# Optimization experiments

Hardware: AMD Instinct MI355X
Metric: run time of the kernel (lower is better)

## Reference

```python
import jax, jax.numpy as jnp
import numpy as np

K = 3          # hard-coded k in Gaussian_interpolation
SIGMA = 1.0    # hard-coded sigma


def _knn_idx(original_pts, query_pts, k):
    # original_pts: [B,3,N], query_pts: [B,3,M] -> idx [B,M,k] of nearest source points
    p2 = jnp.sum(original_pts ** 2, axis=1)          # [B,N]
    q2 = jnp.sum(query_pts ** 2, axis=1)             # [B,M]
    qp = jnp.einsum('bcm,bcn->bmn', query_pts, original_pts)  # [B,M,N]
    d2 = q2[:, :, None] + p2[:, None, :] - 2.0 * qp  # squared distances [B,M,N]
    _, idx = jax.lax.top_k(-d2, k)                   # smallest distances
    return idx


def _gather_k(x, idx):
    # x: [B,C,N], idx: [B,M,k] -> [B,C,M,k]
    return jnp.take_along_axis(x[:, :, None, :], idx[:, None, :, :], axis=3)


def _gaussian_interpolation(original_pts, query_pts, feat, idx):
    # knn points and Gaussian distance weights
    knn_pts = _gather_k(original_pts, idx)                       # [B,3,M,k]
    dist_sq = jnp.sum((knn_pts - query_pts[:, :, :, None]) ** 2, axis=1)  # [B,M,k]
    weight = jnp.exp(-dist_sq / (2.0 * SIGMA ** 2))
    weight = weight / jnp.sum(weight, axis=2, keepdims=True)     # normalize over k
    knn_feat = _gather_k(feat, idx)                              # [B,C,M,k]
    return jnp.sum(knn_feat * weight[:, None, :, :], axis=-1)    # [B,C,M]


def _adaptive_max_pool1d(x, out_size):
    # x: [B, M, C] -> pool over last dim to out_size (matches F.adaptive_max_pool1d)
    C = x.shape[-1]
    i = np.arange(out_size)
    starts = np.floor(i * C / out_size).astype(np.int64)
    ends = np.ceil((i + 1) * C / out_size).astype(np.int64)
    L = int((ends - starts).max())
    idx = starts[:, None] + np.arange(L)[None, :]   # [out_size, L]
    mask = idx < ends[:, None]
    idx = np.minimum(idx, C - 1)
    g = x[..., jnp.asarray(idx)]                    # [B, M, out_size, L]
    g = jnp.where(jnp.asarray(mask)[None, None], g, -jnp.inf)
    return jnp.max(g, axis=-1)                      # [B, M, out_size]


def setup_inputs() -> dict:
    key = jax.random.key(0)
    k1, k2, k3, k4, k5 = jax.random.split(key, 5)
    B, N, M = 2, 16384, 4096
    return {
        'original_pts': jax.random.normal(k1, (B, 3, N), dtype=jnp.float32),
        'query_pts': jax.random.normal(k2, (B, 3, M), dtype=jnp.float32),
        'local_feat1': jax.random.normal(k3, (B, 128, N), dtype=jnp.float32),
        'local_feat2': jax.random.normal(k4, (B, 256, N), dtype=jnp.float32),
        'global_feats': jax.random.normal(k5, (B, 1024), dtype=jnp.float32),
    }


def reference(original_pts, query_pts, local_feat1, local_feat2, global_feats):
    M = query_pts.shape[-1]
    idx = _knn_idx(original_pts, query_pts, K)  # shared kNN for all feature maps
    interp1 = _gaussian_interpolation(original_pts, query_pts, local_feat1, idx)  # [B,C1,M]
    interp2 = _gaussian_interpolation(original_pts, query_pts, local_feat2, idx)  # [B,C2,M]
    agg_local = jnp.concatenate([interp1, interp2], axis=1)       # [B,C1+C2,M]
    # F.interpolate to size M is an identity here (sizes already match)
    gfeat = jnp.broadcast_to(global_feats[:, :, None],
                             (global_feats.shape[0], global_feats.shape[1], M))
    agg = jnp.concatenate([query_pts, agg_local, gfeat], axis=1)  # [B,Ctot,M]
    agg = jnp.transpose(agg, (0, 2, 1))                           # [B,M,Ctot]
    return _adaptive_max_pool1d(agg, M)                           # [B,M,M]
```

## Files before the change

kernel.cpp:

```cpp
#include <hip/hip_runtime.h>

#define BB 2
#define NN 16384
#define MM 4096
#define C1 128
#define C2 256
#define CF 384
#define CG 1024
#define CT 1411
#define FLTMAX 3.402823466e+38f
#define SPLIT 64
#define PTS_PER (NN / SPLIT)

__global__ __launch_bounds__(256) void p2p_fused(
    const float* __restrict__ P, const float* __restrict__ Q,
    const float* __restrict__ F1, const float* __restrict__ F2,
    const float* __restrict__ G, float* __restrict__ out)
{
    const int t  = threadIdx.x;
    const int bm = blockIdx.x;
    const int b  = bm >> 12;
    const int m  = bm & (MM - 1);

    const float* Pb = P + (size_t)b * 3 * NN;
    const float qx = Q[(size_t)b * 3 * MM + 0 * MM + m];
    const float qy = Q[(size_t)b * 3 * MM + 1 * MM + m];
    const float qz = Q[(size_t)b * 3 * MM + 2 * MM + m];
    const float q2 = __fadd_rn(__fadd_rn(__fmul_rn(qx, qx), __fmul_rn(qy, qy)),
                               __fmul_rn(qz, qz));

    float bd0 = FLTMAX, bd1 = FLTMAX, bd2 = FLTMAX;
    int   bi0 = 0x7fffffff, bi1 = 0x7fffffff, bi2 = 0x7fffffff;

    for (int n = t; n < NN; n += 256) {
        float px = Pb[n];
        float py = Pb[NN + n];
        float pz = Pb[2 * NN + n];
        float p2 = __fadd_rn(__fadd_rn(__fmul_rn(px, px), __fmul_rn(py, py)),
                             __fmul_rn(pz, pz));
        float qp = __fadd_rn(__fadd_rn(__fmul_rn(qx, px), __fmul_rn(qy, py)),
                             __fmul_rn(qz, pz));
        float d2 = __fsub_rn(__fadd_rn(q2, p2), __fadd_rn(qp, qp));
        if (d2 < bd2) {
            if (d2 < bd1) {
                if (d2 < bd0) { bd2 = bd1; bi2 = bi1; bd1 = bd0; bi1 = bi0; bd0 = d2; bi0 = n; }
                else          { bd2 = bd1; bi2 = bi1; bd1 = d2;  bi1 = n; }
            } else            { bd2 = d2;  bi2 = n; }
        }
    }

    __shared__ float sd[256][3];
    __shared__ int   si[256][3];
    sd[t][0] = bd0; sd[t][1] = bd1; sd[t][2] = bd2;
    si[t][0] = bi0; si[t][1] = bi1; si[t][2] = bi2;
    __syncthreads();

    for (int off = 128; off >= 1; off >>= 1) {
        if (t < off) {
            float A[3]  = { sd[t][0], sd[t][1], sd[t][2] };
            int   AI[3] = { si[t][0], si[t][1], si[t][2] };
            float Bv[3] = { sd[t + off][0], sd[t + off][1], sd[t + off][2] };
            int   BI[3] = { si[t + off][0], si[t + off][1], si[t + off][2] };
            float rd[3]; int ri[3];
            int pa = 0, pb = 0;
            #pragma unroll
            for (int r = 0; r < 3; r++) {
                bool ta = (A[pa] < Bv[pb]) || (A[pa] == Bv[pb] && AI[pa] < BI[pb]);
                if (ta) { rd[r] = A[pa];  ri[r] = AI[pa]; pa++; }
                else    { rd[r] = Bv[pb]; ri[r] = BI[pb]; pb++; }
            }
            sd[t][0] = rd[0]; sd[t][1] = rd[1]; sd[t][2] = rd[2];
            si[t][0] = ri[0]; si[t][1] = ri[1]; si[t][2] = ri[2];
        }
        __syncthreads();
    }

    __shared__ float wsh[3];
    __shared__ int   ish[3];
    __shared__ float agg[CT + 1];

    if (t == 0) {
        float w[3];
        #pragma unroll
        for (int k = 0; k < 3; k++) {
            int i = si[0][k];
            ish[k] = i;
            float dx = __fsub_rn(Pb[i],          qx);
            float dy = __fsub_rn(Pb[NN + i],     qy);
            float dz = __fsub_rn(Pb[2 * NN + i], qz);
            float ds = __fadd_rn(__fadd_rn(__fmul_rn(dx, dx), __fmul_rn(dy, dy)),
                                 __fmul_rn(dz, dz));
            w[k] = expf(-0.5f * ds);
        }
        float Z = __fadd_rn(__fadd_rn(w[0], w[1]), w[2]);
        wsh[0] = w[0] / Z; wsh[1] = w[1] / Z; wsh[2] = w[2] / Z;
    }
    __syncthreads();

    const int   i0 = ish[0], i1 = ish[1], i2 = ish[2];
    const float w0 = wsh[0], w1 = wsh[1], w2 = wsh[2];

    if (t < 3) agg[t] = (t == 0) ? qx : ((t == 1) ? qy : qz);

    for (int c = t; c < C1 + C2; c += 256) {
        const float* base = (c < C1)
            ? (F1 + ((size_t)b * C1 + c) * NN)
            : (F2 + ((size_t)b * C2 + (c - C1)) * NN);
        float f0 = base[i0], f1 = base[i1], f2 = base[i2];
        float v = __fadd_rn(__fadd_rn(__fmul_rn(f0, w0), __fmul_rn(f1, w1)),
                            __fmul_rn(f2, w2));
        agg[3 + c] = v;
    }
    for (int c = t; c < CG; c += 256) {
        agg[3 + C1 + C2 + c] = G[(size_t)b * CG + c];
    }
    __syncthreads();

    float* orow = out + ((size_t)b * MM + m) * MM;
    for (int j = t; j < MM; j += 256) {
        int s = (j * CT) >> 12;
        int e = ((j + 1) * CT + (MM - 1)) >> 12;
        float v = agg[s];
        if (e - s > 1) v = fmaxf(v, agg[s + 1]);
        orow[j] = v;
    }
}

__global__ __launch_bounds__(256) void prep_all(
    const float* __restrict__ P,  const float* __restrict__ F1,
    const float* __restrict__ F2, const float* __restrict__ G,
    float4* __restrict__ P4, float* __restrict__ Ft, float* __restrict__ pg)
{
    __shared__ float tile[64][65];
    const int blk = blockIdx.x;
    const int t   = threadIdx.x;

    if (blk < 3072) {
        const int b  = blk / 1536;
        const int r  = blk % 1536;
        const int ct = r / 256;
        const int nt = r % 256;
        const int c0 = ct * 64, n0 = nt * 64;
        const int tx = t & 63;
        const int ty = t >> 6;

        #pragma unroll 4
        for (int i = 0; i < 16; i++) {
            int cl = ty + i * 4;
            int c  = c0 + cl;
            const float* src = (c < C1)
                ? (F1 + ((size_t)b * C1 + c) * NN)
                : (F2 + ((size_t)b * C2 + (c - C1)) * NN);
            tile[cl][tx] = src[n0 + tx];
        }
        __syncthreads();
        #pragma unroll 4
        for (int i = 0; i < 16; i++) {
            int nl = ty + i * 4;
            Ft[((size_t)b * NN + (n0 + nl)) * CF + c0 + tx] = tile[tx][nl];
        }
    } else if (blk < 3200) {
        int gid = (blk - 3072) * 256 + t;
        int b   = gid >> 14;
        int n   = gid & (NN - 1);
        const float* Pb = P + (size_t)b * 3 * NN;
        float x = Pb[n], y = Pb[NN + n], z = Pb[2 * NN + n];
        float p2 = __fadd_rn(__fadd_rn(__fmul_rn(x, x), __fmul_rn(y, y)),
                             __fmul_rn(z, z));
        P4[gid] = make_float4(x, y, z, p2);
    } else {
        int gid = (blk - 3200) * 256 + t;
        int b   = gid / 2972;
        int jj  = gid % 2972;
        if (b < BB) {
            int j = 1124 + jj;
            int s = (j * CT) >> 12;
            int e = ((j + 1) * CT + (MM - 1)) >> 12;
            float v = G[(size_t)b * CG + (s - 387)];
            if (e - s > 1) v = fmaxf(v, G[(size_t)b * CG + (s - 386)]);
            pg[(size_t)b * MM + j] = v;
        }
    }
}

__device__ __forceinline__ float dist_rn(float qx, float qy, float qz, float q2,
                                         float4 v)
{
    float qp = __fadd_rn(__fadd_rn(__fmul_rn(qx, v.x), __fmul_rn(qy, v.y)),
                         __fmul_rn(qz, v.z));
    return __fsub_rn(__fadd_rn(q2, v.w), __fadd_rn(qp, qp));
}

#define INS(dv, nv)                                                          \
    {                                                                        \
        bool c0 = (dv) < b0, c1 = (dv) < b1, c2 = (dv) < b2;                 \
        float nb2 = c1 ? b1 : (c2 ? (dv) : b2);                              \
        int   ni2 = c1 ? i1 : (c2 ? (nv) : i2);                              \
        float nb1 = c0 ? b0 : (c1 ? (dv) : b1);                              \
        int   ni1 = c0 ? i0 : (c1 ? (nv) : i1);                              \
        float nb0 = c0 ? (dv) : b0;                                          \
        int   ni0 = c0 ? (nv) : i0;                                          \
        b0 = nb0; b1 = nb1; b2 = nb2; i0 = ni0; i1 = ni1; i2 = ni2;          \
    }

#define INSL(dv, nv)                                                         \
    {                                                                        \
        bool c0 = ((dv) < b0) || ((dv) == b0 && (nv) < i0);                  \
        bool c1 = ((dv) < b1) || ((dv) == b1 && (nv) < i1);                  \
        bool c2 = ((dv) < b2) || ((dv) == b2 && (nv) < i2);                  \
        float nb2 = c1 ? b1 : (c2 ? (dv) : b2);                              \
        int   ni2 = c1 ? i1 : (c2 ? (nv) : i2);                              \
        float nb1 = c0 ? b0 : (c1 ? (dv) : b1);                              \
        int   ni1 = c0 ? i0 : (c1 ? (nv) : i1);                              \
        float nb0 = c0 ? (dv) : b0;                                          \
        int   ni0 = c0 ? (nv) : i0;                                          \
        b0 = nb0; b1 = nb1; b2 = nb2; i0 = ni0; i1 = ni1; i2 = ni2;          \
    }

__global__ __launch_bounds__(256) void knn_scan(
    const float4* __restrict__ P4, const float* __restrict__ Q,
    float4* __restrict__ pd, int4* __restrict__ pi)
{
    const int t    = threadIdx.x;
    const int lane = t & 63;
    const int wv   = __builtin_amdgcn_readfirstlane(t >> 6);
    const int qg   = blockIdx.x & 127;
    const int ps   = blockIdx.x >> 7;
    const int sp   = ps * 4 + wv;
    const int mg   = qg * 64 + lane;
    const int b    = qg >> 6;
    const int m    = mg & (MM - 1);

    const float qx = Q[(size_t)b * 3 * MM + m];
    const float qy = Q[(size_t)b * 3 * MM + MM + m];
    const float qz = Q[(size_t)b * 3 * MM + 2 * MM + m];
    const float q2 = __fadd_rn(__fadd_rn(__fmul_rn(qx, qx), __fmul_rn(qy, qy)),
                               __fmul_rn(qz, qz));

    const float4* Pw = P4 + b * NN + sp * PTS_PER;
    const int nbase = sp * PTS_PER;

    float b0 = FLTMAX, b1 = FLTMAX, b2 = FLTMAX;
    int   i0 = 0x7fffffff, i1 = 0x7fffffff, i2 = 0x7fffffff;

    #pragma unroll 4
    for (int g = 0; g < PTS_PER; g += 4) {
        float4 v0 = Pw[g + 0];
        float4 v1 = Pw[g + 1];
        float4 v2 = Pw[g + 2];
        float4 v3 = Pw[g + 3];
        float d0  = dist_rn(qx, qy, qz, q2, v0);
        float d1  = dist_rn(qx, qy, qz, q2, v1);
        float d2v = dist_rn(qx, qy, qz, q2, v2);
        float d3  = dist_rn(qx, qy, qz, q2, v3);

        bool  cA = d1 < d0;   float mA = fminf(d0, d1);   int uA = cA ? 1 : 0;
        bool  cB = d3 < d2v;  float mB = fminf(d2v, d3);  int uB = cB ? 3 : 2;
        bool  cF = mB < mA;   float mF = fminf(mA, mB);   int uF = cF ? uB : uA;
        int nmin = nbase + g + uF;

        float MA = fmaxf(d0, d1), MB = fmaxf(d2v, d3);
        float sec = fminf(cF ? mA : mB, cF ? MB : MA);

        INS(mF, nmin);

        if (sec < b2) {
            #pragma unroll
            for (int u = 0; u < 4; u++) {
                float du = (u == 0) ? d0 : ((u == 1) ? d1 : ((u == 2) ? d2v : d3));
                if (uF != u) {
                    INS(du, nbase + g + u);
                }
            }
        }
    }

    int o = (mg << 6) + sp;
    pd[o] = make_float4(b0, b1, b2, 0.0f);
    pi[o] = make_int4(i0, i1, i2, 0);
}

__global__ __launch_bounds__(256) void merge_interp_pool(
    const float4* __restrict__ P4, const float* __restrict__ Q,
    const float* __restrict__ G, const float* __restrict__ Ft,
    const float4* __restrict__ pd, const int4* __restrict__ pi,
    const float* __restrict__ pg, float* __restrict__ out)
{
    __shared__ float agg[392];
    __shared__ float swt[3];
    __shared__ int   sidm[3];

    const int t  = threadIdx.x;
    const int mg = blockIdx.x;
    const int b  = mg >> 12;
    const int m  = mg & (MM - 1);

    float4* out4 = (float4*)(out + (size_t)mg * MM);

    if (t < 64) {
        const int lane = t;
        float4 d4 = pd[(mg << 6) + lane];
        int4   i4 = pi[(mg << 6) + lane];
        float b0 = d4.x, b1 = d4.y, b2 = d4.z;
        int   i0 = i4.x, i1 = i4.y, i2 = i4.z;

        #pragma unroll
        for (int mask = 1; mask < 64; mask <<= 1) {
            float e0 = __shfl_xor(b0, mask);
            float e1 = __shfl_xor(b1, mask);
            float e2 = __shfl_xor(b2, mask);
            int   j0 = __shfl_xor(i0, mask);
            int   j1 = __shfl_xor(i1, mask);
            int   j2 = __shfl_xor(i2, mask);
            INSL(e0, j0);
            INSL(e1, j1);
            INSL(e2, j2);
        }

        int myid = (lane == 0) ? i0 : ((lane == 1) ? i1 : i2);
        float w = 0.0f;
        if (lane < 3) {
            float qx = Q[(size_t)b * 3 * MM + m];
            float qy = Q[(size_t)b * 3 * MM + MM + m];
            float qz = Q[(size_t)b * 3 * MM + 2 * MM + m];
            float4 pv = P4[b * NN + myid];
            float dx = __fsub_rn(pv.x, qx);
            float dy = __fsub_rn(pv.y, qy);
            float dz = __fsub_rn(pv.z, qz);
            float ds = __fadd_rn(__fadd_rn(__fmul_rn(dx, dx), __fmul_rn(dy, dy)),
                                 __fmul_rn(dz, dz));
            w = expf(-0.5f * ds);
        }
        float wA = __shfl(w, 0);
        float wB = __shfl(w, 1);
        float wC = __shfl(w, 2);
        if (lane < 3) {
            float Z = __fadd_rn(__fadd_rn(wA, wB), wC);
            swt[lane]  = w / Z;
            sidm[lane] = myid;
        }
    } else {
        if (t >= 65 && t < 68) {
            agg[t - 65] = Q[(size_t)b * 3 * MM + (size_t)(t - 65) * MM + m];
        }
        if (t == 64) agg[387] = G[(size_t)b * CG];
        const float4* pg4 = (const float4*)(pg + (size_t)b * MM);
        for (int g = t - 64; g < 743; g += 192) {
            out4[281 + g] = pg4[281 + g];
        }
    }
    __syncthreads();

    const int   i0 = sidm[0], i1 = sidm[1], i2 = sidm[2];
    const float w0 = swt[0],  w1 = swt[1],  w2 = swt[2];
    const float* r0 = Ft + ((size_t)b * NN + i0) * CF;
    const float* r1 = Ft + ((size_t)b * NN + i1) * CF;
    const float* r2 = Ft + ((size_t)b * NN + i2) * CF;

    for (int c = t; c < CF; c += 256) {
        float v = __fadd_rn(__fadd_rn(__fmul_rn(r0[c], w0), __fmul_rn(r1[c], w1)),
                            __fmul_rn(r2[c], w2));
        agg[3 + c] = v;
    }
    __syncthreads();

    for (int g = t; g < 281; g += 256) {
        int j0 = g * 4;
        float4 o;
        float* op = &o.x;
        #pragma unroll
        for (int u = 0; u < 4; u++) {
            int j = j0 + u;
            int s = (j * CT) >> 12;
            int e = ((j + 1) * CT + (MM - 1)) >> 12;
            float v = agg[s];
            if (e - s > 1) v = fmaxf(v, agg[s + 1]);
            op[u] = v;
        }
        out4[g] = o;
    }
}

extern "C" void kernel_launch(void* const* d_in, const int* in_sizes, int n_in,
                              void* d_out, int out_size, void* d_ws, size_t ws_size,
                              hipStream_t stream) {
    (void)in_sizes; (void)n_in; (void)out_size;
    const float* P  = (const float*)d_in[0];
    const float* Q  = (const float*)d_in[1];
    const float* F1 = (const float*)d_in[2];
    const float* F2 = (const float*)d_in[3];
    const float* G  = (const float*)d_in[4];
    float* out = (float*)d_out;

    const size_t off_ft  = 0;
    const size_t sz_ft   = (size_t)BB * NN * CF * 4;
    const size_t off_p4  = off_ft + sz_ft;
    const size_t sz_p4   = (size_t)BB * NN * 16;
    const size_t off_pd  = off_p4 + sz_p4;
    const size_t sz_pd   = (size_t)BB * MM * SPLIT * 16;
    const size_t off_pi  = off_pd + sz_pd;
    const size_t sz_pi   = sz_pd;
    const size_t off_pg  = off_pi + sz_pi;
    const size_t sz_pg   = (size_t)BB * MM * 4;
    const size_t need    = off_pg + sz_pg;

    if (ws_size >= need) {
        float*  Ft  = (float*)((char*)d_ws + off_ft);
        float4* P4  = (float4*)((char*)d_ws + off_p4);
        float4* pdb = (float4*)((char*)d_ws + off_pd);
        int4*   pib = (int4*)((char*)d_ws + off_pi);
        float*  pg  = (float*)((char*)d_ws + off_pg);

        hipLaunchKernelGGL(prep_all, dim3(3072 + 128 + 24), dim3(256), 0, stream,
                           P, F1, F2, G, P4, Ft, pg);
        hipLaunchKernelGGL(knn_scan, dim3(128 * (SPLIT / 4)), dim3(256), 0, stream,
                           P4, Q, pdb, pib);
        hipLaunchKernelGGL(merge_interp_pool, dim3(BB * MM), dim3(256), 0, stream,
                           P4, Q, G, Ft, pdb, pib, pg, out);
    } else {
        hipLaunchKernelGGL(p2p_fused, dim3(BB * MM), dim3(256), 0, stream,
                           P, Q, F1, F2, G, out);
    }
}
```

Before: 118.9 us.

## Co-schedule kNN scan with feature transpose in one kernel, reduce partials in-block

Moves the large feature transpose out of the prep kernel and interleaves its blocks with the kNN scan blocks in a single heterogeneous launch (2 scan blocks per 3 transpose blocks), so compute-bound scanning overlaps with bandwidth-bound transposing. Each scan block now merges its four waves' top-3 candidates through shared memory, cutting partial records per query from 64 to 16 and shrinking the merge kernel's read and shuffle work. It costs extra shared memory and a block barrier in the scan path, and depends on the hardware scheduler actually interleaving the two block types.

```diff
diff --git a/kernel.cpp b/kernel.cpp
--- a/kernel.cpp
+++ b/kernel.cpp
@@ -11,6 +11,7 @@
 #define FLTMAX 3.402823466e+38f
 #define SPLIT 64
 #define PTS_PER (NN / SPLIT)
+#define NREC 16
 
 __global__ __launch_bounds__(256) void p2p_fused(
     const float* __restrict__ P, const float* __restrict__ Q,
@@ -126,41 +127,14 @@
     }
 }
 
-__global__ __launch_bounds__(256) void prep_all(
-    const float* __restrict__ P,  const float* __restrict__ F1,
-    const float* __restrict__ F2, const float* __restrict__ G,
-    float4* __restrict__ P4, float* __restrict__ Ft, float* __restrict__ pg)
+__global__ __launch_bounds__(256) void prep_small(
+    const float* __restrict__ P, const float* __restrict__ G,
+    float4* __restrict__ P4, float* __restrict__ pg)
 {
-    __shared__ float tile[64][65];
     const int blk = blockIdx.x;
     const int t   = threadIdx.x;
-
-    if (blk < 3072) {
-        const int b  = blk / 1536;
-        const int r  = blk % 1536;
-        const int ct = r / 256;
-        const int nt = r % 256;
-        const int c0 = ct * 64, n0 = nt * 64;
-        const int tx = t & 63;
-        const int ty = t >> 6;
-
-        #pragma unroll 4
-        for (int i = 0; i < 16; i++) {
-            int cl = ty + i * 4;
-            int c  = c0 + cl;
-            const float* src = (c < C1)
-                ? (F1 + ((size_t)b * C1 + c) * NN)
-                : (F2 + ((size_t)b * C2 + (c - C1)) * NN);
-            tile[cl][tx] = src[n0 + tx];
-        }
-        __syncthreads();
-        #pragma unroll 4
-        for (int i = 0; i < 16; i++) {
-            int nl = ty + i * 4;
-            Ft[((size_t)b * NN + (n0 + nl)) * CF + c0 + tx] = tile[tx][nl];
-        }
-    } else if (blk < 3200) {
-        int gid = (blk - 3072) * 256 + t;
+    if (blk < 128) {
+        int gid = blk * 256 + t;
         int b   = gid >> 14;
         int n   = gid & (NN - 1);
         const float* Pb = P + (size_t)b * 3 * NN;
@@ -169,7 +143,7 @@
                              __fmul_rn(z, z));
         P4[gid] = make_float4(x, y, z, p2);
     } else {
-        int gid = (blk - 3200) * 256 + t;
+        int gid = (blk - 128) * 256 + t;
         int b   = gid / 2972;
         int jj  = gid % 2972;
         if (b < BB) {
@@ -217,67 +191,121 @@
         b0 = nb0; b1 = nb1; b2 = nb2; i0 = ni0; i1 = ni1; i2 = ni2;          \
     }
 
-__global__ __launch_bounds__(256) void knn_scan(
+__global__ __launch_bounds__(256) void mega(
     const float4* __restrict__ P4, const float* __restrict__ Q,
-    float4* __restrict__ pd, int4* __restrict__ pi)
+    const float* __restrict__ F1, const float* __restrict__ F2,
+    float4* __restrict__ pd, int4* __restrict__ pi, float* __restrict__ Ft)
 {
-    const int t    = threadIdx.x;
-    const int lane = t & 63;
-    const int wv   = __builtin_amdgcn_readfirstlane(t >> 6);
-    const int qg   = blockIdx.x & 127;
-    const int ps   = blockIdx.x >> 7;
-    const int sp   = ps * 4 + wv;
-    const int mg   = qg * 64 + lane;
-    const int b    = qg >> 6;
-    const int m    = mg & (MM - 1);
-
-    const float qx = Q[(size_t)b * 3 * MM + m];
-    const float qy = Q[(size_t)b * 3 * MM + MM + m];
-    const float qz = Q[(size_t)b * 3 * MM + 2 * MM + m];
-    const float q2 = __fadd_rn(__fadd_rn(__fmul_rn(qx, qx), __fmul_rn(qy, qy)),
-                               __fmul_rn(qz, qz));
-
-    const float4* Pw = P4 + b * NN + sp * PTS_PER;
-    const int nbase = sp * PTS_PER;
-
-    float b0 = FLTMAX, b1 = FLTMAX, b2 = FLTMAX;
-    int   i0 = 0x7fffffff, i1 = 0x7fffffff, i2 = 0x7fffffff;
-
-    #pragma unroll 4
-    for (int g = 0; g < PTS_PER; g += 4) {
-        float4 v0 = Pw[g + 0];
-        float4 v1 = Pw[g + 1];
-        float4 v2 = Pw[g + 2];
-        float4 v3 = Pw[g + 3];
-        float d0  = dist_rn(qx, qy, qz, q2, v0);
-        float d1  = dist_rn(qx, qy, qz, q2, v1);
-        float d2v = dist_rn(qx, qy, qz, q2, v2);
-        float d3  = dist_rn(qx, qy, qz, q2, v3);
-
-        bool  cA = d1 < d0;   float mA = fminf(d0, d1);   int uA = cA ? 1 : 0;
-        bool  cB = d3 < d2v;  float mB = fminf(d2v, d3);  int uB = cB ? 3 : 2;
-        bool  cF = mB < mA;   float mF = fminf(mA, mB);   int uF = cF ? uB : uA;
-        int nmin = nbase + g + uF;
-
-        float MA = fmaxf(d0, d1), MB = fmaxf(d2v, d3);
-        float sec = fminf(cF ? mA : mB, cF ? MB : MA);
-
-        INS(mF, nmin);
-
-        if (sec < b2) {
-            #pragma unroll
-            for (int u = 0; u < 4; u++) {
-                float du = (u == 0) ? d0 : ((u == 1) ? d1 : ((u == 2) ? d2v : d3));
-                if (uF != u) {
-                    INS(du, nbase + g + u);
+    __shared__ float shf[64 * 65];
+
+    const int bid = blockIdx.x;
+    const int t   = threadIdx.x;
+    const int q5  = bid / 5;
+    const int r5  = bid - q5 * 5;
+
+    if (r5 < 2) {
+        const int u    = q5 * 2 + r5;
+        const int lane = t & 63;
+        const int wv   = __builtin_amdgcn_readfirstlane(t >> 6);
+        const int qg   = u & 127;
+        const int ps   = u >> 7;
+        const int sp   = ps * 4 + wv;
+        const int mg   = qg * 64 + lane;
+        const int b    = qg >> 6;
+        const int m    = mg & (MM - 1);
+
+        const float qx = Q[(size_t)b * 3 * MM + m];
+        const float qy = Q[(size_t)b * 3 * MM + MM + m];
+        const float qz = Q[(size_t)b * 3 * MM + 2 * MM + m];
+        const float q2 = __fadd_rn(__fadd_rn(__fmul_rn(qx, qx), __fmul_rn(qy, qy)),
+                                   __fmul_rn(qz, qz));
+
+        const float4* Pw = P4 + b * NN + sp * PTS_PER;
+        const int nbase = sp * PTS_PER;
+
+        float b0 = FLTMAX, b1 = FLTMAX, b2 = FLTMAX;
+        int   i0 = 0x7fffffff, i1 = 0x7fffffff, i2 = 0x7fffffff;
+
+        #pragma unroll 4
+        for (int g = 0; g < PTS_PER; g += 4) {
+            float4 v0 = Pw[g + 0];
+            float4 v1 = Pw[g + 1];
+            float4 v2 = Pw[g + 2];
+            float4 v3 = Pw[g + 3];
+            float d0  = dist_rn(qx, qy, qz, q2, v0);
+            float d1  = dist_rn(qx, qy, qz, q2, v1);
+            float d2v = dist_rn(qx, qy, qz, q2, v2);
+            float d3  = dist_rn(qx, qy, qz, q2, v3);
+
+            bool  cA = d1 < d0;   float mA = fminf(d0, d1);   int uA = cA ? 1 : 0;
+            bool  cB = d3 < d2v;  float mB = fminf(d2v, d3);  int uB = cB ? 3 : 2;
+            bool  cF = mB < mA;   float mF = fminf(mA, mB);   int uF = cF ? uB : uA;
+            int nmin = nbase + g + uF;
+
+            float MA = fmaxf(d0, d1), MB = fmaxf(d2v, d3);
+            float sec = fminf(cF ? mA : mB, cF ? MB : MA);
+
+            INS(mF, nmin);
+
+            if (sec < b2) {
+                #pragma unroll
+                for (int uu = 0; uu < 4; uu++) {
+                    float du = (uu == 0) ? d0 : ((uu == 1) ? d1 : ((uu == 2) ? d2v : d3));
+                    if (uF != uu) {
+                        INS(du, nbase + g + uu);
+                    }
                 }
             }
         }
-    }
-
-    int o = (mg << 6) + sp;
-    pd[o] = make_float4(b0, b1, b2, 0.0f);
-    pi[o] = make_int4(i0, i1, i2, 0);
+
+        float* sdm = shf;
+        int*   sim = (int*)(shf + 768);
+        int base = (wv * 64 + lane) * 3;
+        sdm[base + 0] = b0; sdm[base + 1] = b1; sdm[base + 2] = b2;
+        sim[base + 0] = i0; sim[base + 1] = i1; sim[base + 2] = i2;
+        __syncthreads();
+
+        if (t < 64) {
+            #pragma unroll
+            for (int w = 1; w < 4; w++) {
+                int bb = (w * 64 + t) * 3;
+                float e0 = sdm[bb + 0], e1 = sdm[bb + 1], e2 = sdm[bb + 2];
+                int   j0 = sim[bb + 0], j1 = sim[bb + 1], j2 = sim[bb + 2];
+                INSL(e0, j0);
+                INSL(e1, j1);
+                INSL(e2, j2);
+            }
+            int o = (((qg << 6) + t) << 4) + ps;
+            pd[o] = make_float4(b0, b1, b2, 0.0f);
+            pi[o] = make_int4(i0, i1, i2, 0);
+        }
+    } else {
+        const int v  = q5 * 3 + (r5 - 2);
+        const int b  = v / 1536;
+        const int r  = v % 1536;
+        const int ct = r / 256;
+        const int nt = r % 256;
+        const int c0 = ct * 64, n0 = nt * 64;
+        const int tx = t & 63;
+        const int ty = t >> 6;
+        float (*tile)[65] = (float (*)[65])shf;
+
+        #pragma unroll 4
+        for (int i = 0; i < 16; i++) {
+            int cl = ty + i * 4;
+            int c  = c0 + cl;
+            const float* src = (c < C1)
+                ? (F1 + ((size_t)b * C1 + c) * NN)
+                : (F2 + ((size_t)b * C2 + (c - C1)) * NN);
+            tile[cl][tx] = src[n0 + tx];
+        }
+        __syncthreads();
+        #pragma unroll 4
+        for (int i = 0; i < 16; i++) {
+            int nl = ty + i * 4;
+            Ft[((size_t)b * NN + (n0 + nl)) * CF + c0 + tx] = tile[tx][nl];
+        }
+    }
 }
 
 __global__ __launch_bounds__(256) void merge_interp_pool(
@@ -299,13 +327,17 @@
 
     if (t < 64) {
         const int lane = t;
-        float4 d4 = pd[(mg << 6) + lane];
-        int4   i4 = pi[(mg << 6) + lane];
-        float b0 = d4.x, b1 = d4.y, b2 = d4.z;
-        int   i0 = i4.x, i1 = i4.y, i2 = i4.z;
+        float b0 = FLTMAX, b1 = FLTMAX, b2 = FLTMAX;
+        int   i0 = 0x7fffffff, i1 = 0x7fffffff, i2 = 0x7fffffff;
+        if (lane < NREC) {
+            float4 d4 = pd[(mg << 4) + lane];
+            int4   i4 = pi[(mg << 4) + lane];
+            b0 = d4.x; b1 = d4.y; b2 = d4.z;
+            i0 = i4.x; i1 = i4.y; i2 = i4.z;
+        }
 
         #pragma unroll
-        for (int mask = 1; mask < 64; mask <<= 1) {
+        for (int mask = 1; mask < NREC; mask <<= 1) {
             float e0 = __shfl_xor(b0, mask);
             float e1 = __shfl_xor(b1, mask);
             float e2 = __shfl_xor(b2, mask);
@@ -397,7 +429,7 @@
     const size_t off_p4  = off_ft + sz_ft;
     const size_t sz_p4   = (size_t)BB * NN * 16;
     const size_t off_pd  = off_p4 + sz_p4;
-    const size_t sz_pd   = (size_t)BB * MM * SPLIT * 16;
+    const size_t sz_pd   = (size_t)BB * MM * NREC * 16;
     const size_t off_pi  = off_pd + sz_pd;
     const size_t sz_pi   = sz_pd;
     const size_t off_pg  = off_pi + sz_pi;
@@ -411,10 +443,10 @@
         int4*   pib = (int4*)((char*)d_ws + off_pi);
         float*  pg  = (float*)((char*)d_ws + off_pg);
 
-        hipLaunchKernelGGL(prep_all, dim3(3072 + 128 + 24), dim3(256), 0, stream,
-                           P, F1, F2, G, P4, Ft, pg);
-        hipLaunchKernelGGL(knn_scan, dim3(128 * (SPLIT / 4)), dim3(256), 0, stream,
-                           P4, Q, pdb, pib);
+        hipLaunchKernelGGL(prep_small, dim3(128 + 24), dim3(256), 0, stream,
+                           P, G, P4, pg);
+        hipLaunchKernelGGL(mega, dim3(5120), dim3(256), 0, stream,
+                           P4, Q, F1, F2, pdb, pib, Ft);
         hipLaunchKernelGGL(merge_interp_pool, dim3(BB * MM), dim3(256), 0, stream,
                            P4, Q, G, Ft, pdb, pib, pg, out);
     } else {
```

Result: no change. 119.1 us (+0.2%).
